# Optimization experiments

Hardware: AMD Instinct MI355X
Metric: run time of the kernel (lower is better)

The kernel has to match this reference:

```python
import jax, jax.numpy as jnp
import numpy as np

D_CONV = 4
D_STATE = 32
DT_RANK = 16


def setup_inputs() -> dict:
    key = jax.random.key(0)
    ks = jax.random.split(key, 12)
    B, D, L, DI = 4, 256, 1024, 256
    s = 0.02
    return {
        "x": jax.random.normal(ks[0], (B, D, L), jnp.float32),
        "Win": jax.random.normal(ks[1], (4, D, 2 * DI), jnp.float32) * s,
        "Wconv": jax.random.normal(ks[2], (4, DI, D_CONV), jnp.float32) * 0.2,
        "bconv": jnp.zeros((4, DI), jnp.float32),
        "Wxp": jax.random.normal(ks[3], (4, DI, DT_RANK + 2 * D_STATE), jnp.float32) * s,
        "Wdt": jax.random.normal(ks[4], (4, DT_RANK, DI), jnp.float32) * s,
        "bdt": jnp.full((4, DI), -2.0, jnp.float32),
        "Alog": jnp.tile(jnp.log(jnp.arange(1, D_STATE + 1, dtype=jnp.float32))[None, None, :], (4, DI, 1)),
        "Dskip": jnp.ones((4, DI), jnp.float32),
        "Wout": jax.random.normal(ks[5], (4, DI, D), jnp.float32) * s,
        "Wg": jax.random.normal(ks[6], (2, L, L), jnp.float32) * 0.01,
        "bg": jnp.zeros((2, L), jnp.float32),
        "alpha": jnp.ones((2,), jnp.float32),
        "gamma": jnp.ones((2, L), jnp.float32),
        "beta": jnp.zeros((2, L), jnp.float32),
    }


def _selective_scan(u, dt, Bm, Cm, A):
    # u, dt: [B,L,di]; Bm, Cm: [B,L,N]; A: [di,N]
    dBu = dt * u
    def step(h, inp):
        dt_t, dbu_t, B_t, C_t = inp  # [B,di],[B,di],[B,N],[B,N]
        h = jnp.exp(dt_t[:, :, None] * A) * h + dbu_t[:, :, None] * B_t[:, None, :]
        y = jnp.einsum('bdn,bn->bd', h, C_t)
        return h, y
    xs = (jnp.moveaxis(dt, 1, 0), jnp.moveaxis(dBu, 1, 0),
          jnp.moveaxis(Bm, 1, 0), jnp.moveaxis(Cm, 1, 0))
    h0 = jnp.zeros((u.shape[0], A.shape[0], A.shape[1]), u.dtype)
    _, ys = jax.lax.scan(step, h0, xs)  # ys: [L,B,di]
    return jnp.moveaxis(ys, 0, 1)


def _mamba_layer(x_bdl, Win, Wconv, bconv, Wxp, Wdt, bdt, Alog, Dskip, Wout):
    x = jnp.swapaxes(x_bdl, 1, 2)  # [B,L,D]
    L = x.shape[1]
    u, z = jnp.split(x @ Win, 2, axis=-1)  # each [B,L,di]
    up = jnp.pad(u, ((0, 0), (D_CONV - 1, 0), (0, 0)))
    u = sum(up[:, k:k + L, :] * Wconv[:, k] for k in range(D_CONV)) + bconv
    u = jax.nn.silu(u)
    proj = u @ Wxp
    dtp = proj[..., :DT_RANK]
    Bm = proj[..., DT_RANK:DT_RANK + D_STATE]
    Cm = proj[..., DT_RANK + D_STATE:]
    dt = jax.nn.softplus(dtp @ Wdt + bdt)
    y = _selective_scan(u, dt, Bm, Cm, -jnp.exp(Alog)) + u * Dskip
    y = y * jax.nn.silu(z)
    return jnp.swapaxes(y @ Wout, 1, 2)  # [B,d_out,L]


def _forward(x, Win, Wconv, bconv, Wxp, Wdt, bdt, Alog, Dskip, Wout, Wg, bg, alpha, gamma, beta):
    def branch(inp, i0, i1, j):
        h = _mamba_layer(inp, Win[i0], Wconv[i0], bconv[i0], Wxp[i0], Wdt[i0], bdt[i0], Alog[i0], Dskip[i0], Wout[i0])
        h = _mamba_layer(h, Win[i1], Wconv[i1], bconv[i1], Wxp[i1], Wdt[i1], bdt[i1], Alog[i1], Dskip[i1], Wout[i1])
        return gamma[j] * jnp.tanh(alpha[j] * h) + beta[j]  # DyTanh over last dim
    def gate(j):
        return jax.nn.sigmoid(jnp.einsum('bdl,ml->bdm', x, Wg[j]) + bg[j])
    m = branch(x, 0, 1, 0) * gate(0)
    rx = jnp.flip(x, axis=-1)
    rm = branch(rx, 2, 3, 1) * gate(1)
    return m + jnp.flip(rm, axis=-1)


def reference(x, Win, Wconv, bconv, Wxp, Wdt, bdt, Alog, Dskip, Wout, Wg, bg, alpha, gamma, beta):
    return _forward(x, Win, Wconv, bconv, Wxp, Wdt, bdt, Alog, Dskip, Wout, Wg, bg, alpha, gamma, beta)
```

## Files before the change

kernel.cpp:

```cpp
#include <hip/hip_runtime.h>


#define LSEQ 1024
#define SCAN_CL 16
#define SCAN_NC 64

#if __has_builtin(__builtin_amdgcn_exp2f)
#define EXP2(x) __builtin_amdgcn_exp2f(x)
#else
#define EXP2(x) exp2f(x)
#endif

typedef short bf16x8 __attribute__((ext_vector_type(8)));
typedef float f32x4 __attribute__((ext_vector_type(4)));

__device__ __forceinline__ float sigmoidf_(float x) { return 1.f / (1.f + __expf(-x)); }
__device__ __forceinline__ float siluf_(float x)    { return x / (1.f + __expf(-x)); }
__device__ __forceinline__ float softplusf_(float x){ return x > 20.f ? x : log1pf(__expf(x)); }

__device__ __forceinline__ unsigned short bf16rne_(float v) {
  unsigned u = __float_as_uint(v);
  return (unsigned short)((u + 0x7FFFu + ((u >> 16) & 1u)) >> 16);
}
__device__ __forceinline__ float bfto_(unsigned short h) {
  return __uint_as_float(((unsigned)h) << 16);
}
__device__ __forceinline__ void split3_(float v, unsigned short& h,
                                        unsigned short& m, unsigned short& l) {
  h = bf16rne_(v); float r = v - bfto_(h);
  m = bf16rne_(r); float r2 = r - bfto_(m);
  l = bf16rne_(r2);
}

__device__ __forceinline__ long swzi(long idx, long row) {
  return idx ^ (((row >> 1) & 3) << 3);
}

__device__ void tconv3_body(const float* __restrict__ in,
                            unsigned short* __restrict__ oh,
                            unsigned short* __restrict__ om,
                            unsigned short* __restrict__ ol,
                            int K, int N, int bx, int by, int z) {
  __shared__ float T[32][33];
  int n0 = bx * 32, k0 = by * 32;
  int tx = threadIdx.x & 31, ty = threadIdx.x >> 5;
  const float* src = in + (long)z * K * N;
#pragma unroll
  for (int m = 0; m < 4; ++m)
    T[ty + 8 * m][tx] = src[(long)(k0 + ty + 8 * m) * N + n0 + tx];
  __syncthreads();
  long obase = (long)z * N * K;
#pragma unroll
  for (int m = 0; m < 4; ++m) {
    float v = T[tx][ty + 8 * m];
    int n = n0 + ty + 8 * m;
    long o = swzi(obase + (long)n * K + k0 + tx, n);
    split3_(v, oh[o], om[o], ol[o]);
  }
}

__device__ void split3v_body(const float4* __restrict__ in,
                             unsigned short* __restrict__ oh,
                             unsigned short* __restrict__ om,
                             unsigned short* __restrict__ ol, int i) {
  float4 v = in[i];
  long b = 4L * i;
  long sb = swzi(b, b >> 10);
  ushort4 H, M, L;
  split3_(v.x, H.x, M.x, L.x); split3_(v.y, H.y, M.y, L.y);
  split3_(v.z, H.z, M.z, L.z); split3_(v.w, H.w, M.w, L.w);
  *(ushort4*)(oh + sb) = H; *(ushort4*)(om + sb) = M; *(ushort4*)(ol + sb) = L;
}

__global__ __launch_bounds__(256)
void preprocess_kernel(const float* __restrict__ x, const float* __restrict__ Wg,
                       const float* __restrict__ Win, const float* __restrict__ Wout,
                       const float* __restrict__ Alog,
                       unsigned short* __restrict__ Xh, unsigned short* __restrict__ Xm,
                       unsigned short* __restrict__ Xl,
                       unsigned short* __restrict__ XGh, unsigned short* __restrict__ XGm,
                       unsigned short* __restrict__ XGl,
                       unsigned short* __restrict__ Wgh, unsigned short* __restrict__ Wgm,
                       unsigned short* __restrict__ Wgl,
                       unsigned short* __restrict__ WinTh, unsigned short* __restrict__ WinTm,
                       unsigned short* __restrict__ WinTl,
                       unsigned short* __restrict__ WoutTh, unsigned short* __restrict__ WoutTm,
                       unsigned short* __restrict__ WoutTl,
                       float* __restrict__ Aneg) {
  const int bid = blockIdx.x;
  if (bid < 8192) {
    long idx = (long)bid * 256 + threadIdx.x;
    int d = (int)(idx & 255);
    long t = idx >> 8;
    int l = (int)(t & 1023);
    int t2 = (int)(t >> 10);
    int b = t2 & 3;
    int j = t2 >> 2;
    int lsrc = j ? (1023 - l) : l;
    float v = x[((long)(b * 256 + d)) * LSEQ + lsrc];
    long o = swzi(idx, t);
    split3_(v, Xh[o], Xm[o], Xl[o]);
  } else if (bid < 9216) {
    int i = (bid - 8192) * 256 + threadIdx.x;
    split3v_body((const float4*)x, XGh, XGm, XGl, i);
  } else if (bid < 11264) {
    int i = (bid - 9216) * 256 + threadIdx.x;
    split3v_body((const float4*)Wg, Wgh, Wgm, Wgl, i);
  } else if (bid < 11776) {
    int t = bid - 11264;
    tconv3_body(Win, WinTh, WinTm, WinTl, 256, 512, t & 15, (t >> 4) & 7, t >> 7);
  } else if (bid < 12032) {
    int t = bid - 11776;
    tconv3_body(Wout, WoutTh, WoutTm, WoutTl, 256, 256, t & 7, (t >> 3) & 7, t >> 6);
  } else {
    int idx = (bid - 12032) * 256 + threadIdx.x;
    Aneg[idx] = -__expf(Alog[idx]) * 1.4426950408889634f;
  }
}

__device__ __forceinline__ void gload16(const unsigned short* g, unsigned short* l) {
  __builtin_amdgcn_global_load_lds(
      (const __attribute__((address_space(1))) unsigned int*)g,
      (__attribute__((address_space(3))) unsigned int*)l, 16, 0, 0);
}

template <int KSPLIT>
__global__ __launch_bounds__(256)
void gemm_mfma(const unsigned short* __restrict__ Ah_g,
               const unsigned short* __restrict__ Am_g,
               const unsigned short* __restrict__ Al_g, long aZ, int lda,
               const unsigned short* __restrict__ Bh_g,
               const unsigned short* __restrict__ Bm_g,
               const unsigned short* __restrict__ Bl_g, long bZ, int ldb,
               float* __restrict__ C, long cZ, int N, int KH) {
  __shared__ unsigned short S[2][6][128 * 32];
  const int bz = blockIdx.z;
  const int z  = (KSPLIT == 2) ? (bz >> 1) : bz;
  const int kh = (KSPLIT == 2) ? (bz & 1) : 0;
  const int m0 = blockIdx.y * 128, n0 = blockIdx.x * 128;
  const int tid = threadIdx.x;

  const long khoff = (long)kh * KH;
  const long a0 = (long)z * aZ + (long)(m0 + (tid >> 2)) * lda + khoff + (tid & 3) * 8;
  const long a1 = a0 + 64L * lda;
  const long b0 = (long)z * bZ + (long)(n0 + (tid >> 2)) * ldb + khoff + (tid & 3) * 8;
  const long b1 = b0 + 64L * ldb;
  const int l0 = tid * 8, l1 = tid * 8 + 2048;

  const int lane = tid & 63, w = tid >> 6;
  const int wr = w >> 1, wc = w & 1;
  const int fr = lane & 15, g = lane >> 4;

  f32x4 acc[4][4];
#pragma unroll
  for (int i = 0; i < 4; ++i)
#pragma unroll
    for (int j = 0; j < 4; ++j)
#pragma unroll
      for (int q = 0; q < 4; ++q) acc[i][j][q] = 0.f;

#define ISSUE_TILE(B, KOFF)                                 \
  do {                                                      \
    gload16(Ah_g + a0 + (KOFF), &S[B][0][l0]);              \
    gload16(Ah_g + a1 + (KOFF), &S[B][0][l1]);              \
    gload16(Am_g + a0 + (KOFF), &S[B][1][l0]);              \
    gload16(Am_g + a1 + (KOFF), &S[B][1][l1]);              \
    gload16(Al_g + a0 + (KOFF), &S[B][2][l0]);              \
    gload16(Al_g + a1 + (KOFF), &S[B][2][l1]);              \
    gload16(Bh_g + b0 + (KOFF), &S[B][3][l0]);              \
    gload16(Bh_g + b1 + (KOFF), &S[B][3][l1]);              \
    gload16(Bm_g + b0 + (KOFF), &S[B][4][l0]);              \
    gload16(Bm_g + b1 + (KOFF), &S[B][4][l1]);              \
    gload16(Bl_g + b0 + (KOFF), &S[B][5][l0]);              \
    gload16(Bl_g + b1 + (KOFF), &S[B][5][l1]);              \
  } while (0)

  ISSUE_TILE(0, 0);
  int cur = 0;

  for (int k0 = 0; k0 < KH; k0 += 32) {
    asm volatile("s_waitcnt lgkmcnt(0)" ::: "memory");
    __builtin_amdgcn_s_barrier();
    if (k0 + 32 < KH) {
      ISSUE_TILE(cur ^ 1, k0 + 32);
      asm volatile("s_waitcnt vmcnt(12)" ::: "memory");
    } else {
      asm volatile("s_waitcnt vmcnt(0)" ::: "memory");
    }
    __builtin_amdgcn_s_barrier();
    __builtin_amdgcn_sched_barrier(0);

    bf16x8 fb[3][4];
#pragma unroll
    for (int nf = 0; nf < 4; ++nf) {
      int rb = wc * 64 + nf * 16 + fr;
      int ob = rb * 32 + ((g ^ ((rb >> 1) & 3)) << 3);
      fb[0][nf] = *(const bf16x8*)&S[cur][3][ob];
      fb[1][nf] = *(const bf16x8*)&S[cur][4][ob];
      fb[2][nf] = *(const bf16x8*)&S[cur][5][ob];
    }
#pragma unroll
    for (int mf = 0; mf < 4; ++mf) {
      int ra = wr * 64 + mf * 16 + fr;
      int oa = ra * 32 + ((g ^ ((ra >> 1) & 3)) << 3);
      bf16x8 fah = *(const bf16x8*)&S[cur][0][oa];
      bf16x8 fam = *(const bf16x8*)&S[cur][1][oa];
      bf16x8 fal = *(const bf16x8*)&S[cur][2][oa];
#pragma unroll
      for (int nf = 0; nf < 4; ++nf) {
        acc[mf][nf] = __builtin_amdgcn_mfma_f32_16x16x32_bf16(fah, fb[0][nf], acc[mf][nf], 0, 0, 0);
        acc[mf][nf] = __builtin_amdgcn_mfma_f32_16x16x32_bf16(fah, fb[1][nf], acc[mf][nf], 0, 0, 0);
        acc[mf][nf] = __builtin_amdgcn_mfma_f32_16x16x32_bf16(fam, fb[0][nf], acc[mf][nf], 0, 0, 0);
        acc[mf][nf] = __builtin_amdgcn_mfma_f32_16x16x32_bf16(fam, fb[1][nf], acc[mf][nf], 0, 0, 0);
        acc[mf][nf] = __builtin_amdgcn_mfma_f32_16x16x32_bf16(fah, fb[2][nf], acc[mf][nf], 0, 0, 0);
        acc[mf][nf] = __builtin_amdgcn_mfma_f32_16x16x32_bf16(fal, fb[0][nf], acc[mf][nf], 0, 0, 0);
      }
    }
    cur ^= 1;
  }
#undef ISSUE_TILE

  float* Cz = C + (long)bz * cZ;
#pragma unroll
  for (int mf = 0; mf < 4; ++mf)
#pragma unroll
    for (int nf = 0; nf < 4; ++nf) {
      int col = n0 + wc * 64 + nf * 16 + fr;
      int row0 = m0 + wr * 64 + mf * 16 + g * 4;
#pragma unroll
      for (int q = 0; q < 4; ++q)
        Cz[(long)(row0 + q) * N + col] = acc[mf][nf][q];
    }
}

template <int OP>
__global__ __launch_bounds__(256)
void combine2_kernel(const float* __restrict__ P, long pz,
                     const float* __restrict__ bias, int nmask,
                     float* __restrict__ outF,
                     unsigned short* __restrict__ oh,
                     unsigned short* __restrict__ om,
                     unsigned short* __restrict__ ol, long oz) {
  int z = blockIdx.y;
  long i = (long)blockIdx.x * 256 + threadIdx.x;
  float v = P[(long)(2 * z) * pz + i] + P[(long)(2 * z + 1) * pz + i];
  if (OP == 1) {
    outF[(long)z * oz + i] = sigmoidf_(v + bias[z * (nmask + 1) + (int)(i & nmask)]);
  } else {
    long o = (long)z * oz + swzi(i, i >> 8);
    split3_(v, oh[o], om[o], ol[o]);
  }
}

__global__ __launch_bounds__(256)
void gemm23_kernel(const float* __restrict__ UC, const float* __restrict__ Wxp,
                   const float* __restrict__ Wdt, const float* __restrict__ bdt,
                   float* __restrict__ PROJ, float* __restrict__ DTo, int stage) {
  __shared__ float As[16][17];
  __shared__ float Ws[16][80];
  __shared__ float PR[16][17];
  __shared__ float WD[16][256];
  const int z = blockIdx.y;
  const int lidx = stage + 2 * z;
  const int m0 = blockIdx.x * 16;
  const long abase = (long)z * 4096 * 256 + (long)m0 * 256;
  const float* W = Wxp + (long)lidx * 256 * 80;
  const int tid = threadIdx.x;
  const int tx = tid & 15, ty = tid >> 4;

#pragma unroll
  for (int t = 0; t < 16; ++t) {
    int e = t * 256 + tid;
    WD[e >> 8][e & 255] = Wdt[(long)lidx * 4096 + e];
  }

  float acc[5];
#pragma unroll
  for (int j = 0; j < 5; ++j) acc[j] = 0.f;

  for (int k0 = 0; k0 < 256; k0 += 16) {
    As[tx][ty] = UC[abase + (long)ty * 256 + k0 + tx];
    {
      int k = tid >> 4, cg2 = (tid & 15) * 5;
#pragma unroll
      for (int i2 = 0; i2 < 5; ++i2)
        Ws[k][cg2 + i2] = W[(long)(k0 + k) * 80 + cg2 + i2];
    }
    __syncthreads();
#pragma unroll
    for (int kk = 0; kk < 16; ++kk) {
      float a = As[kk][ty];
#pragma unroll
      for (int j = 0; j < 5; ++j)
        acc[j] = fmaf(a, Ws[kk][tx * 5 + j], acc[j]);
    }
    __syncthreads();
  }

#pragma unroll
  for (int j = 0; j < 5; ++j) {
    int c = tx * 5 + j;
    float v = acc[j];
    PROJ[((long)z * 4096 + m0 + ty) * 80 + c] = v;
    if (c < 16) PR[ty][c] = v;
  }
  __syncthreads();

  for (int it = 0; it < 16; ++it) {
    float ssum = 0.f;
#pragma unroll
    for (int k = 0; k < 16; ++k) ssum = fmaf(PR[it][k], WD[k][tid], ssum);
    DTo[((long)z * 4096 + m0 + it) * 256 + tid] =
        softplusf_(ssum + bdt[lidx * 256 + tid]);
  }
}

__global__ __launch_bounds__(256) void conv_kernel(const float* __restrict__ UZ,
                                                   const float* __restrict__ Wconv,
                                                   const float* __restrict__ bconv,
                                                   float* __restrict__ uc, int stage) {
  long idx = (long)blockIdx.x * 256 + threadIdx.x;
  int di = (int)(idx & 255);
  long r = idx >> 8;
  int l = (int)(r & 1023);
  int j = (int)(r >> 12);
  int lidx = stage + 2 * j;
  const float* wc = Wconv + (long)(lidx * 256 + di) * 4;
  float acc = bconv[lidx * 256 + di];
  const float* up = UZ + (r - 3) * 512 + di;
  if (l >= 3) {
    acc = fmaf(up[0], wc[0], acc);
    acc = fmaf(up[512], wc[1], acc);
    acc = fmaf(up[1024], wc[2], acc);
    acc = fmaf(up[1536], wc[3], acc);
  } else {
    for (int k = 3 - l; k < 4; ++k) acc = fmaf(up[(long)k * 512], wc[k], acc);
  }
  uc[idx] = acc * sigmoidf_(acc);
}

template <int PASS>
__global__ __launch_bounds__(256)
void scan_chunk_kernel(const float* __restrict__ dt,
                       const float* __restrict__ uc,
                       const float* __restrict__ UZ,
                       const float* __restrict__ proj,
                       const float* __restrict__ Aneg,
                       const float* __restrict__ Dskip,
                       float* __restrict__ HST,
                       float* __restrict__ DTS,
                       unsigned short* __restrict__ YGh,
                       unsigned short* __restrict__ YGm,
                       unsigned short* __restrict__ YGl, int stage) {
  __shared__ __align__(16) float BC[SCAN_CL][64];
  const int blk = blockIdx.x;
  const int chunk = blk & (SCAN_NC - 1);
  const int jb = blk >> 6;
  const int di = threadIdx.x;
  const int j = jb >> 2;
  const int lidx = stage + 2 * j;
  const long r0 = (long)jb * 1024 + (long)chunk * SCAN_CL;

  for (int e = threadIdx.x; e < SCAN_CL * 64; e += 256) {
    int l = e >> 6, col = e & 63;
    BC[l][col] = proj[(r0 + l) * 80 + 16 + col];
  }

  float A[32];
  {
    const float4* ap = (const float4*)(Aneg + ((long)(lidx * 256 + di)) * 32);
#pragma unroll
    for (int q = 0; q < 8; ++q) {
      float4 v = ap[q];
      A[4 * q] = v.x; A[4 * q + 1] = v.y; A[4 * q + 2] = v.z; A[4 * q + 3] = v.w;
    }
  }

  const long sbase = (((long)jb * SCAN_NC + chunk) * 256 + di) * 32;
  float h[32];
  if (PASS == 0) {
#pragma unroll
    for (int n = 0; n < 32; ++n) h[n] = 0.f;
  } else {
    const float4* hp = (const float4*)(HST + sbase);
#pragma unroll
    for (int q = 0; q < 8; ++q) {
      float4 v = hp[q];
      h[4 * q] = v.x; h[4 * q + 1] = v.y; h[4 * q + 2] = v.z; h[4 * q + 3] = v.w;
    }
  }

  float Dsk = 0.f, dtsum = 0.f;
  if (PASS == 1) Dsk = Dskip[lidx * 256 + di];

  const float* dtp = dt + r0 * 256 + di;
  const float* up  = uc + r0 * 256 + di;
  const float* zp  = UZ + r0 * 512 + 256 + di;

  __syncthreads();

  float Db[2][8], Ub[2][8], Zb[2][8];
#pragma unroll
  for (int i = 0; i < 8; ++i) {
    Db[0][i] = dtp[(long)i * 256];
    Ub[0][i] = up[(long)i * 256];
    if (PASS == 1) Zb[0][i] = zp[(long)i * 512];
  }

#pragma unroll
  for (int bt = 0; bt < SCAN_CL / 8; ++bt) {
    const int cur = bt & 1, nxt = cur ^ 1;
    if (bt < SCAN_CL / 8 - 1) {
#pragma unroll
      for (int i = 0; i < 8; ++i) {
        long l = (long)(bt + 1) * 8 + i;
        Db[nxt][i] = dtp[l * 256];
        Ub[nxt][i] = up[l * 256];
        if (PASS == 1) Zb[nxt][i] = zp[l * 512];
      }
    }
#pragma unroll
    for (int i = 0; i < 8; ++i) {
      const int l = bt * 8 + i;
      float dtv = Db[cur][i];
      float uv  = Ub[cur][i];
      float du  = dtv * uv;
      if (PASS == 0) dtsum += dtv;
      float yacc[4] = {0.f, 0.f, 0.f, 0.f};
      const float4* bc4 = (const float4*)&BC[l][0];
#pragma unroll
      for (int q = 0; q < 8; ++q) {
        float4 bv = bc4[q];
        float4 cv = bc4[8 + q];
        const float* bp = &bv.x;
        const float* cp = &cv.x;
#pragma unroll
        for (int k = 0; k < 4; ++k) {
          int n = 4 * q + k;
          float a = EXP2(dtv * A[n]);
          h[n] = fmaf(a, h[n], du * bp[k]);
          yacc[n & 3] = fmaf(h[n], cp[k], yacc[n & 3]);
        }
      }
      if (PASS == 1) {
        float y = (yacc[0] + yacc[1]) + (yacc[2] + yacc[3]);
        float zv = Zb[cur][i];
        float val = (y + uv * Dsk) * siluf_(zv);
        long o = swzi((r0 + l) * 256 + di, r0 + l);
        split3_(val, YGh[o], YGm[o], YGl[o]);
      }
    }
  }

  if (PASS == 0) {
    float4* hp = (float4*)(HST + sbase);
#pragma unroll
    for (int q = 0; q < 8; ++q)
      hp[q] = make_float4(h[4 * q], h[4 * q + 1], h[4 * q + 2], h[4 * q + 3]);
    DTS[((long)jb * SCAN_NC + chunk) * 256 + di] = dtsum;
  }
}

__global__ __launch_bounds__(256)
void scan_combine_kernel(float* __restrict__ HST, const float* __restrict__ DTS,
                         const float* __restrict__ Aneg, int stage) {
  int t = blockIdx.x * 256 + threadIdx.x;
  int n = t & 31;
  int di = (t >> 5) & 255;
  int jb = t >> 13;
  int lidx = stage + 2 * (jb >> 2);
  float A = Aneg[((long)(lidx * 256 + di)) * 32 + n];
  float hs = 0.f;
  for (int cb = 0; cb < SCAN_NC; cb += 8) {
    float s[8], P[8], hv[8];
#pragma unroll
    for (int i = 0; i < 8; ++i) {
      long base = ((long)jb * SCAN_NC + cb + i) * 256 + di;
      s[i] = HST[base * 32 + n];
      P[i] = DTS[base];
    }
#pragma unroll
    for (int i = 0; i < 8; ++i) P[i] = EXP2(A * P[i]);
#pragma unroll
    for (int i = 0; i < 8; ++i) {
      hv[i] = hs;
      hs = fmaf(P[i], hs, s[i]);
    }
#pragma unroll
    for (int i = 0; i < 8; ++i) {
      long base = ((long)jb * SCAN_NC + cb + i) * 256 + di;
      HST[base * 32 + n] = hv[i];
    }
  }
}

__global__ __launch_bounds__(256) void combine_kernel(const float* __restrict__ PG,
                                                      long pz,
                                                      const float* __restrict__ gate,
                                                      const float* __restrict__ alpha,
                                                      const float* __restrict__ gamma,
                                                      const float* __restrict__ beta,
                                                      float* __restrict__ out) {
  long idx = (long)blockIdx.x * 256 + threadIdx.x;
  int l = (int)(idx & 1023);
  long t = idx >> 10;
  int d = (int)(t & 255);
  int b = (int)(t >> 8);
  int lr = 1023 - l;
  long b0 = ((long)(b * 1024 + l)) * 256 + d;
  long b1 = ((long)(b * 1024 + lr)) * 256 + d;
  float h0 = PG[b0] + PG[pz + b0];
  float h1 = PG[2 * pz + b1] + PG[3 * pz + b1];
  float g0 = gate[((long)(b * 256 + d)) * 1024 + l];
  float g1 = gate[(long)1024 * 1024 + ((long)(b * 256 + d)) * 1024 + lr];
  float m0 = (gamma[l] * tanhf(alpha[0] * h0) + beta[l]) * g0;
  float m1 = (gamma[1024 + lr] * tanhf(alpha[1] * h1) + beta[1024 + lr]) * g1;
  out[idx] = m0 + m1;
}

extern "C" void kernel_launch(void* const* d_in, const int* in_sizes, int n_in,
                              void* d_out, int out_size, void* d_ws, size_t ws_size,
                              hipStream_t stream) {
  const float* x     = (const float*)d_in[0];
  const float* Win   = (const float*)d_in[1];
  const float* Wconv = (const float*)d_in[2];
  const float* bconv = (const float*)d_in[3];
  const float* Wxp   = (const float*)d_in[4];
  const float* Wdt   = (const float*)d_in[5];
  const float* bdt   = (const float*)d_in[6];
  const float* Alog  = (const float*)d_in[7];
  const float* Dskip = (const float*)d_in[8];
  const float* Wout  = (const float*)d_in[9];
  const float* Wg    = (const float*)d_in[10];
  const float* bg    = (const float*)d_in[11];
  const float* alpha = (const float*)d_in[12];
  const float* gamma = (const float*)d_in[13];
  const float* beta  = (const float*)d_in[14];
  float* out = (float*)d_out;

  float* ws   = (float*)d_ws;
  float* UZ   = ws;
  float* UC   = UZ + 4194304;
  float* PROJ = UC + 2097152;
  float* DT   = PROJ + 655360;
  float* GATE = DT + 2097152;
  float* ANEG = GATE + 2097152;
  float* HST  = ANEG + 32768;
  float* DTS  = HST + 4194304;
  float* PG   = DTS + 131072;
  unsigned short* Xpl  = (unsigned short*)(PG + 4194304);
  unsigned short* YGpl = Xpl + 3 * 2097152;
  unsigned short* XGpl = YGpl + 3 * 2097152;
  unsigned short* Wgpl = XGpl + 3 * 1048576;
  unsigned short* WinT = Wgpl + 3 * 2097152;
  unsigned short* WoutT = WinT + 3 * 524288;
  unsigned short* Xh = Xpl, *Xm = Xpl + 2097152, *Xl = Xpl + 2 * 2097152;
  unsigned short* YGh = YGpl, *YGm = YGpl + 2097152, *YGl = YGpl + 2 * 2097152;
  unsigned short* XGh = XGpl, *XGm = XGpl + 1048576, *XGl = XGpl + 2 * 1048576;
  unsigned short* Wgh = Wgpl, *Wgm = Wgpl + 2097152, *Wgl = Wgpl + 2 * 2097152;
  unsigned short* WinTh = WinT, *WinTm = WinT + 524288, *WinTl = WinT + 2 * 524288;
  unsigned short* WoutTh = WoutT, *WoutTm = WoutT + 262144, *WoutTl = WoutT + 2 * 262144;

  preprocess_kernel<<<dim3(12160), dim3(256), 0, stream>>>(
      x, Wg, Win, Wout, Alog, Xh, Xm, Xl, XGh, XGm, XGl,
      Wgh, Wgm, Wgl, WinTh, WinTm, WinTl, WoutTh, WoutTm, WoutTl, ANEG);

  gemm_mfma<2><<<dim3(8, 8, 4), dim3(256), 0, stream>>>(
      XGh, XGm, XGl, 0L, 1024,
      Wgh, Wgm, Wgl, (long)1024 * 1024, 1024,
      PG, (long)1024 * 1024, 1024, 512);
  combine2_kernel<1><<<dim3(4096, 2), dim3(256), 0, stream>>>(
      PG, (long)1024 * 1024, bg, 1023, GATE, nullptr, nullptr, nullptr,
      (long)1024 * 1024);

  for (int s = 0; s < 2; ++s) {
    gemm_mfma<1><<<dim3(4, 32, 2), dim3(256), 0, stream>>>(
        Xh, Xm, Xl, (long)4096 * 256, 256,
        WinTh + (long)s * 131072, WinTm + (long)s * 131072, WinTl + (long)s * 131072,
        (long)262144, 256,
        UZ, (long)4096 * 512, 512, 256);

    conv_kernel<<<dim3(8192), dim3(256), 0, stream>>>(UZ, Wconv, bconv, UC, s);

    gemm23_kernel<<<dim3(256, 2), dim3(256), 0, stream>>>(
        UC, Wxp, Wdt, bdt, PROJ, DT, s);

    scan_chunk_kernel<0><<<dim3(8 * SCAN_NC), dim3(256), 0, stream>>>(
        DT, UC, UZ, PROJ, ANEG, Dskip, HST, DTS, YGh, YGm, YGl, s);
    scan_combine_kernel<<<dim3(256), dim3(256), 0, stream>>>(HST, DTS, ANEG, s);
    scan_chunk_kernel<1><<<dim3(8 * SCAN_NC), dim3(256), 0, stream>>>(
        DT, UC, UZ, PROJ, ANEG, Dskip, HST, DTS, YGh, YGm, YGl, s);

    gemm_mfma<2><<<dim3(2, 32, 4), dim3(256), 0, stream>>>(
        YGh, YGm, YGl, (long)4096 * 256, 256,
        WoutTh + (long)s * 65536, WoutTm + (long)s * 65536, WoutTl + (long)s * 65536,
        (long)131072, 256,
        PG, (long)4096 * 256, 256, 128);
    if (s == 0) {
      combine2_kernel<2><<<dim3(4096, 2), dim3(256), 0, stream>>>(
          PG, (long)4096 * 256, nullptr, 0, nullptr, Xh, Xm, Xl, (long)4096 * 256);
    }
  }

  combine_kernel<<<dim3(4096), dim3(256), 0, stream>>>(
      PG, (long)4096 * 256, GATE, alpha, gamma, beta, out);
}
```

Measured before the change: 307.7 us.

## Triple-buffer GEMM LDS tiles and hoist all scan chunk loads upfront

The MFMA GEMM moves from double to triple buffering in LDS, so loads run two tiles ahead and the wait allows 24 outstanding loads. This is meant to hide more global latency. LDS use per block rises from about 96KB to 144KB, which may reduce occupancy to one block per CU. The scan kernel now issues all 16 timesteps of dt/u/z loads before reading A and h, replacing the two-stage register prefetch. This exposes more memory-level parallelism at the cost of more live registers.

```diff
diff --git a/kernel.cpp b/kernel.cpp
--- a/kernel.cpp
+++ b/kernel.cpp
@@ -133,7 +133,7 @@
                const unsigned short* __restrict__ Bm_g,
                const unsigned short* __restrict__ Bl_g, long bZ, int ldb,
                float* __restrict__ C, long cZ, int N, int KH) {
-  __shared__ unsigned short S[2][6][128 * 32];
+  __shared__ unsigned short S[3][6][128 * 32];
   const int bz = blockIdx.z;
   const int z  = (KSPLIT == 2) ? (bz >> 1) : bz;
   const int kh = (KSPLIT == 2) ? (bz & 1) : 0;
@@ -176,13 +176,17 @@
   } while (0)
 
   ISSUE_TILE(0, 0);
+  ISSUE_TILE(1, 32);
   int cur = 0;
 
   for (int k0 = 0; k0 < KH; k0 += 32) {
     asm volatile("s_waitcnt lgkmcnt(0)" ::: "memory");
     __builtin_amdgcn_s_barrier();
-    if (k0 + 32 < KH) {
-      ISSUE_TILE(cur ^ 1, k0 + 32);
+    if (k0 + 64 < KH) {
+      int nb = (cur >= 1) ? cur - 1 : 2;
+      ISSUE_TILE(nb, k0 + 64);
+      asm volatile("s_waitcnt vmcnt(24)" ::: "memory");
+    } else if (k0 + 32 < KH) {
       asm volatile("s_waitcnt vmcnt(12)" ::: "memory");
     } else {
       asm volatile("s_waitcnt vmcnt(0)" ::: "memory");
@@ -216,7 +220,7 @@
         acc[mf][nf] = __builtin_amdgcn_mfma_f32_16x16x32_bf16(fal, fb[0][nf], acc[mf][nf], 0, 0, 0);
       }
     }
-    cur ^= 1;
+    cur = (cur == 2) ? 0 : cur + 1;
   }
 #undef ISSUE_TILE
 
@@ -366,6 +370,19 @@
     BC[l][col] = proj[(r0 + l) * 80 + 16 + col];
   }
 
+  const float* dtp = dt + r0 * 256 + di;
+  const float* up  = uc + r0 * 256 + di;
+  const float* zp  = UZ + r0 * 512 + 256 + di;
+  float Dall[SCAN_CL], Uall[SCAN_CL], Zall[SCAN_CL];
+#pragma unroll
+  for (int i = 0; i < SCAN_CL; ++i) Dall[i] = dtp[(long)i * 256];
+#pragma unroll
+  for (int i = 0; i < SCAN_CL; ++i) Uall[i] = up[(long)i * 256];
+  if (PASS == 1) {
+#pragma unroll
+    for (int i = 0; i < SCAN_CL; ++i) Zall[i] = zp[(long)i * 512];
+  }
+
   float A[32];
   {
     const float4* ap = (const float4*)(Aneg + ((long)(lidx * 256 + di)) * 32);
@@ -393,62 +410,35 @@
   float Dsk = 0.f, dtsum = 0.f;
   if (PASS == 1) Dsk = Dskip[lidx * 256 + di];
 
-  const float* dtp = dt + r0 * 256 + di;
-  const float* up  = uc + r0 * 256 + di;
-  const float* zp  = UZ + r0 * 512 + 256 + di;
-
   __syncthreads();
 
-  float Db[2][8], Ub[2][8], Zb[2][8];
-#pragma unroll
-  for (int i = 0; i < 8; ++i) {
-    Db[0][i] = dtp[(long)i * 256];
-    Ub[0][i] = up[(long)i * 256];
-    if (PASS == 1) Zb[0][i] = zp[(long)i * 512];
-  }
-
-#pragma unroll
-  for (int bt = 0; bt < SCAN_CL / 8; ++bt) {
-    const int cur = bt & 1, nxt = cur ^ 1;
-    if (bt < SCAN_CL / 8 - 1) {
-#pragma unroll
-      for (int i = 0; i < 8; ++i) {
-        long l = (long)(bt + 1) * 8 + i;
-        Db[nxt][i] = dtp[l * 256];
-        Ub[nxt][i] = up[l * 256];
-        if (PASS == 1) Zb[nxt][i] = zp[l * 512];
+#pragma unroll
+  for (int l = 0; l < SCAN_CL; ++l) {
+    float dtv = Dall[l];
+    float uv  = Uall[l];
+    float du  = dtv * uv;
+    if (PASS == 0) dtsum += dtv;
+    float yacc[4] = {0.f, 0.f, 0.f, 0.f};
+    const float4* bc4 = (const float4*)&BC[l][0];
+#pragma unroll
+    for (int q = 0; q < 8; ++q) {
+      float4 bv = bc4[q];
+      float4 cv = bc4[8 + q];
+      const float* bp = &bv.x;
+      const float* cp = &cv.x;
+#pragma unroll
+      for (int k = 0; k < 4; ++k) {
+        int n = 4 * q + k;
+        float a = EXP2(dtv * A[n]);
+        h[n] = fmaf(a, h[n], du * bp[k]);
+        yacc[n & 3] = fmaf(h[n], cp[k], yacc[n & 3]);
       }
     }
-#pragma unroll
-    for (int i = 0; i < 8; ++i) {
-      const int l = bt * 8 + i;
-      float dtv = Db[cur][i];
-      float uv  = Ub[cur][i];
-      float du  = dtv * uv;
-      if (PASS == 0) dtsum += dtv;
-      float yacc[4] = {0.f, 0.f, 0.f, 0.f};
-      const float4* bc4 = (const float4*)&BC[l][0];
-#pragma unroll
-      for (int q = 0; q < 8; ++q) {
-        float4 bv = bc4[q];
-        float4 cv = bc4[8 + q];
-        const float* bp = &bv.x;
-        const float* cp = &cv.x;
-#pragma unroll
-        for (int k = 0; k < 4; ++k) {
-          int n = 4 * q + k;
-          float a = EXP2(dtv * A[n]);
-          h[n] = fmaf(a, h[n], du * bp[k]);
-          yacc[n & 3] = fmaf(h[n], cp[k], yacc[n & 3]);
-        }
-      }
-      if (PASS == 1) {
-        float y = (yacc[0] + yacc[1]) + (yacc[2] + yacc[3]);
-        float zv = Zb[cur][i];
-        float val = (y + uv * Dsk) * siluf_(zv);
-        long o = swzi((r0 + l) * 256 + di, r0 + l);
-        split3_(val, YGh[o], YGm[o], YGl[o]);
-      }
+    if (PASS == 1) {
+      float y = (yacc[0] + yacc[1]) + (yacc[2] + yacc[3]);
+      float val = (y + uv * Dsk) * siluf_(Zall[l]);
+      long o = swzi((r0 + l) * 256 + di, r0 + l);
+      split3_(val, YGh[o], YGm[o], YGl[o]);
     }
   }
 
```

After: 310.9 us. About the same (+1.0%).
